# Kernel optimization log

Hardware: AMD Instinct MI355X
Metric: run time of the kernel (lower is better)

Reference implementation:

```python
import jax, jax.numpy as jnp
import numpy as np

# dims (match init_kwargs / input_specs)
K = 2      # sampling size k
B = 4      # batch
V = 2000   # vocab_size == number of graph nodes
D = 64     # embedding_dim
H = 4      # n_heads
DH = 64    # hidden units per head (n_hidden_units[0])
P = 128    # penultimate_hidden_unit
ALPHA = 0.2
NEG = -9e15  # large negative used by GAT to mask non-edges before softmax


def leaky_relu(v):
    return jnp.where(v >= 0, v, ALPHA * v)


def setup_inputs() -> dict:
    key = jax.random.key(0)
    ks = jax.random.split(key, 10)
    x = (jax.random.uniform(ks[0], (K, B, V)) < 0.1).astype(jnp.float32)
    E = jax.random.normal(ks[1], (V, D))                                 # embedding_weight (normal init)
    W = jax.random.normal(ks[2], (H, D, DH)) * (1.0 / np.sqrt(D))        # per-head GAT weight
    a1 = jax.random.normal(ks[3], (H, DH)) * 0.1                         # attention vec, src half
    a2 = jax.random.normal(ks[4], (H, DH)) * 0.1                         # attention vec, dst half
    cls_w = jax.random.normal(ks[5], (H * DH,))                          # cls_weight
    ac1 = jax.random.normal(ks[6], (H * DH,)) * 0.1                      # CLS attention vec halves
    ac2 = jax.random.normal(ks[7], (H * DH,)) * 0.1
    dense_W = jax.random.normal(ks[8], (H * DH, P)) * (1.0 / np.sqrt(H * DH))
    dense_b = jnp.zeros((P,), dtype=jnp.float32)
    return dict(x=x, E=E, W=W, a1=a1, a2=a2, cls_w=cls_w, ac1=ac1, ac2=ac2,
                dense_W=dense_W, dense_b=dense_b)


def gat_block(feat, mask, W, a1, a2):
    # feat: [B,V,Fin], mask: [B,V,V] bool (adj>0 support from outer product)
    Wh = jnp.einsum('bvf,hfo->bhvo', feat, W)                 # [B,H,V,DH]
    f1 = jnp.einsum('bhvo,ho->bhv', Wh, a1)
    f2 = jnp.einsum('bhvo,ho->bhv', Wh, a2)
    e = leaky_relu(f1[:, :, :, None] + f2[:, :, None, :])     # [B,H,V,V]
    e = jnp.where(mask[:, None, :, :], e, NEG)
    attn = jax.nn.softmax(e, axis=-1)
    out = jax.nn.elu(jnp.einsum('bhvu,bhuo->bhvo', attn, Wh))  # concat=True -> elu
    b, h, v, o = out.shape
    return out.transpose(0, 2, 1, 3).reshape(b, v, h * o)      # concat heads -> [B,V,H*DH]


def reference(x, E, W, a1, a2, cls_w, ac1, ac2, dense_W, dense_b):
    latents = [jnp.broadcast_to(cls_w, (B, cls_w.shape[0]))]   # CLS token per sample
    for i in range(K):
        xi = x[i]                                              # [B,V]
        present = xi > 0
        mask = present[:, :, None] & present[:, None, :]       # adj = outer(x,x) > 0
        feat = xi[:, :, None] * E[None]                        # mask embeddings by presence
        feat = gat_block(feat, mask, W, a1, a2)                # single hidden GAT layer
        latent = xi[:, :, None] * feat                         # [B,V,H*DH]
        latents.append(jnp.max(latent, axis=1))                # max-pool over nodes
    h = jnp.stack(latents, axis=1)                             # [B,K+1,F]
    cls = h[:, 0]
    e = leaky_relu((cls @ ac1)[:, None] + h @ ac2)             # [B,K+1]
    attn = jax.nn.softmax(e, axis=-1)
    pooled = jnp.einsum('bk,bkf->bf', attn, h)                 # CLS attention pooling
    return jax.nn.elu(pooled @ dense_W + dense_b)              # activation(dense(.))
```

## Files before the change

### kernel.cpp

```cpp
#include <hip/hip_runtime.h>
#include <hip/hip_bf16.h>

#define KK 2
#define BB 4
#define VV 2000
#define DD 64
#define HH 4
#define DHH 64
#define PP 128
#define ALPHA_ 0.2f

#define RPB 32
#define YB  8

typedef __attribute__((ext_vector_type(8))) short bf16x8;
typedef __attribute__((ext_vector_type(4))) float f32x4;

__device__ __forceinline__ float lrelu(float z) { return fmaxf(z, ALPHA_ * z); }
__device__ __forceinline__ float elu_(float z)  { return z > 0.f ? z : expm1f(z); }
__device__ __forceinline__ short f2bf(float f) {
  __hip_bfloat16 h = __float2bfloat16(f);
  return *reinterpret_cast<short*>(&h);
}

#define OFF_EW   0
#define OFF_F1   512000
#define OFF_F2   520000
#define OFF_LAT  528000
#define OFF_CNT  530048
#define OFF_S    530056

__global__ __launch_bounds__(256) void k_pre(
    const float* __restrict__ E, const float* __restrict__ W,
    const float* __restrict__ a1, const float* __restrict__ a2,
    const float* __restrict__ x,
    float* __restrict__ EW, float* __restrict__ F1, float* __restrict__ F2,
    int* __restrict__ S, int* __restrict__ cnt, float* __restrict__ lat) {
  const int bid = blockIdx.x;
  const int wave = threadIdx.x >> 6, lane = threadIdx.x & 63;
  if (bid < 2000) {
    const int h = bid / 500;
    const int v = (bid % 500) * 4 + wave;
    bool pres = false;
#pragma unroll
    for (int kb = 0; kb < KK * BB; ++kb) pres |= (x[kb * VV + v] > 0.f);
    if (!pres) return;
    const float* Wh = W + h * DD * DHH;
    const float* Ev = E + v * DD;
    float acc = 0.f;
#pragma unroll 8
    for (int d = 0; d < DD; ++d) acc = fmaf(Ev[d], Wh[d * DHH + lane], acc);
    EW[(h * VV + v) * DHH + lane] = acc;
    float r1 = acc * a1[h * DHH + lane];
    float r2 = acc * a2[h * DHH + lane];
#pragma unroll
    for (int s = 32; s; s >>= 1) { r1 += __shfl_xor(r1, s); r2 += __shfl_xor(r2, s); }
    if (lane == 0) { F1[h * VV + v] = r1; F2[h * VV + v] = r2; }
  } else {
    if (wave != 0) return;
    const int kb = bid - 2000;
    for (int i = lane; i < 256; i += 64) lat[kb * 256 + i] = 0.f;
    const float* xr = x + kb * VV;
    int base = 0;
    for (int t = 0; t * 64 < VV; ++t) {
      const int v = t * 64 + lane;
      const bool f = (v < VV) && (xr[v] > 0.f);
      const unsigned long long m = __ballot(f);
      if (f) {
        const int pos = base + __popcll(m & ((1ull << lane) - 1ull));
        S[kb * VV + pos] = v;
      }
      base += __popcll(m);
    }
    if (lane == 0) cnt[kb] = base;
  }
}

__global__ __launch_bounds__(256) void k_attn(
    const float* __restrict__ EW, const float* __restrict__ F1,
    const float* __restrict__ F2, const int* __restrict__ S,
    const int* __restrict__ cnt, float* __restrict__ lat) {
  __shared__ int   Sl[2048];
  __shared__ float G2l[2048];
  __shared__ float G1l[2048];
  __shared__ float SF1[RPB], SM[RPB], SIV[RPB];

  const int kb = blockIdx.x;
  const int h  = blockIdx.z;
  const int tid = threadIdx.x;
  const int wave = tid >> 6, lane = tid & 63;
  const int n = cnt[kb];
  const int nt = (n + RPB - 1) / RPB;
  if ((int)blockIdx.y >= nt) return;
  const int nup = (n + 31) & ~31;

  const int* Skb = S + kb * VV;
  const float* F2h = F2 + h * VV;
  const float* F1h = F1 + h * VV;
  const float* EWh = EW + (size_t)h * VV * DHH;

  for (int j = tid; j < nup; j += 256) {
    const int v = (j < n) ? Skb[j] : Skb[0];
    Sl[j] = v;
    G2l[j] = (j < n) ? F2h[v] : 0.f;
    G1l[j] = F1h[v];
  }
  __syncthreads();

  const int col = (wave << 4) | (lane & 15);
  const int q   = lane >> 4;
  const float* EWcol = EWh + col;

  for (int tile = blockIdx.y; tile < nt; tile += YB) {
    const int r0w = tile * RPB + wave * 8;
    bool act[8]; float f1r[8];
#pragma unroll
    for (int i = 0; i < 8; ++i) {
      const int r = r0w + i;
      act[i] = r < n;
      f1r[i] = G1l[act[i] ? r : 0];
    }
    float m[8];
#pragma unroll
    for (int i = 0; i < 8; ++i) m[i] = -3.4e38f;
    for (int jb = lane; jb < n; jb += 64) {
      const float g = G2l[jb];
#pragma unroll
      for (int i = 0; i < 8; ++i) m[i] = fmaxf(m[i], lrelu(f1r[i] + g));
    }
#pragma unroll
    for (int s = 32; s; s >>= 1)
#pragma unroll
      for (int i = 0; i < 8; ++i) m[i] = fmaxf(m[i], __shfl_xor(m[i], s));
    float sm[8];
#pragma unroll
    for (int i = 0; i < 8; ++i) sm[i] = 0.f;
    for (int jb = lane; jb < n; jb += 64) {
      const float g = G2l[jb];
#pragma unroll
      for (int i = 0; i < 8; ++i) sm[i] += __expf(lrelu(f1r[i] + g) - m[i]);
    }
#pragma unroll
    for (int s = 32; s; s >>= 1)
#pragma unroll
      for (int i = 0; i < 8; ++i) sm[i] += __shfl_xor(sm[i], s);

    __syncthreads();
    if (lane == 0) {
#pragma unroll
      for (int i = 0; i < 8; ++i) {
        SF1[wave * 8 + i] = f1r[i];
        SM[wave * 8 + i]  = m[i];
        SIV[wave * 8 + i] = act[i] ? (1.f / sm[i]) : 0.f;
      }
    }
    __syncthreads();

    const int rl = lane & 15;
    const float f1a = SF1[rl],      ma = SM[rl],      ia = SIV[rl];
    const float f1b = SF1[16 + rl], mb = SM[16 + rl], ib = SIV[16 + rl];
    f32x4 acc0 = {0.f, 0.f, 0.f, 0.f}, acc1 = {0.f, 0.f, 0.f, 0.f};
    for (int kc = 0; kc < nup; kc += 32) {
      const int kq = kc + q * 8;
      const int4 va = *reinterpret_cast<const int4*>(&Sl[kq]);
      const int4 vb = *reinterpret_cast<const int4*>(&Sl[kq + 4]);
      const float4 ga = *reinterpret_cast<const float4*>(&G2l[kq]);
      const float4 gb = *reinterpret_cast<const float4*>(&G2l[kq + 4]);
      float bv[8];
      bv[0] = EWcol[(size_t)va.x * DHH];
      bv[1] = EWcol[(size_t)va.y * DHH];
      bv[2] = EWcol[(size_t)va.z * DHH];
      bv[3] = EWcol[(size_t)va.w * DHH];
      bv[4] = EWcol[(size_t)vb.x * DHH];
      bv[5] = EWcol[(size_t)vb.y * DHH];
      bv[6] = EWcol[(size_t)vb.z * DHH];
      bv[7] = EWcol[(size_t)vb.w * DHH];
      const float g[8] = {ga.x, ga.y, ga.z, ga.w, gb.x, gb.y, gb.z, gb.w};
      float pa[8], pb[8];
#pragma unroll
      for (int t = 0; t < 8; ++t) {
        const float gt = g[t];
        pa[t] = __expf(lrelu(f1a + gt) - ma) * ia;
        pb[t] = __expf(lrelu(f1b + gt) - mb) * ib;
      }
      if (kc + 32 > n) {
#pragma unroll
        for (int t = 0; t < 8; ++t)
          if (kq + t >= n) { pa[t] = 0.f; pb[t] = 0.f; }
      }
      bf16x8 A0, A1, Bf;
#pragma unroll
      for (int t = 0; t < 8; ++t) {
        A0[t] = f2bf(pa[t]);
        A1[t] = f2bf(pb[t]);
        Bf[t] = f2bf(bv[t]);
      }
      acc0 = __builtin_amdgcn_mfma_f32_16x16x32_bf16(A0, Bf, acc0, 0, 0, 0);
      acc1 = __builtin_amdgcn_mfma_f32_16x16x32_bf16(A1, Bf, acc1, 0, 0, 0);
    }
    float vmax = -3.4e38f;
#pragma unroll
    for (int r = 0; r < 4; ++r) {
      const int row0 = tile * RPB + (q << 2) + r;
      const int row1 = row0 + 16;
      if (row0 < n) vmax = fmaxf(vmax, acc0[r]);
      if (row1 < n) vmax = fmaxf(vmax, acc1[r]);
    }
    if (vmax > 0.f)
      atomicMax(reinterpret_cast<int*>(&lat[kb * 256 + h * DHH + col]),
                __float_as_int(vmax));
  }
}

__global__ __launch_bounds__(256) void k_final(
    const float* __restrict__ cls_w, const float* __restrict__ ac1,
    const float* __restrict__ ac2, const float* __restrict__ dW,
    const float* __restrict__ db, const float* __restrict__ lat,
    float* __restrict__ out) {
  const int b = blockIdx.x;
  const int tid = threadIdx.x;
  const int lane = tid & 63, wave = tid >> 6;
  __shared__ float pooled[256];
  __shared__ float red[4][4];
  const float cw = cls_w[tid];
  const float l0 = lat[(0 * BB + b) * 256 + tid];
  const float l1 = lat[(1 * BB + b) * 256 + tid];
  float t0 = cw * ac1[tid];
  float t1 = cw * ac2[tid];
  float t2 = l0 * ac2[tid];
  float t3 = l1 * ac2[tid];
#pragma unroll
  for (int s = 32; s; s >>= 1) {
    t0 += __shfl_xor(t0, s); t1 += __shfl_xor(t1, s);
    t2 += __shfl_xor(t2, s); t3 += __shfl_xor(t3, s);
  }
  if (lane == 0) { red[wave][0] = t0; red[wave][1] = t1; red[wave][2] = t2; red[wave][3] = t3; }
  __syncthreads();
  const float ca1 = red[0][0] + red[1][0] + red[2][0] + red[3][0];
  const float d0  = red[0][1] + red[1][1] + red[2][1] + red[3][1];
  const float d1  = red[0][2] + red[1][2] + red[2][2] + red[3][2];
  const float d2  = red[0][3] + red[1][3] + red[2][3] + red[3][3];
  const float e0 = lrelu(ca1 + d0), e1 = lrelu(ca1 + d1), e2 = lrelu(ca1 + d2);
  const float mm = fmaxf(e0, fmaxf(e1, e2));
  const float x0 = __expf(e0 - mm), x1 = __expf(e1 - mm), x2 = __expf(e2 - mm);
  const float invs = 1.f / (x0 + x1 + x2);
  pooled[tid] = (x0 * cw + x1 * l0 + x2 * l1) * invs;
  __syncthreads();
  if (tid < PP) {
    float acc = db[tid];
    for (int f = 0; f < 256; ++f) acc = fmaf(pooled[f], dW[f * PP + tid], acc);
    out[b * PP + tid] = elu_(acc);
  }
}

extern "C" void kernel_launch(void* const* d_in, const int* in_sizes, int n_in,
                              void* d_out, int out_size, void* d_ws, size_t ws_size,
                              hipStream_t stream) {
  const float* x     = (const float*)d_in[0];
  const float* E     = (const float*)d_in[1];
  const float* W     = (const float*)d_in[2];
  const float* a1    = (const float*)d_in[3];
  const float* a2    = (const float*)d_in[4];
  const float* cls_w = (const float*)d_in[5];
  const float* ac1   = (const float*)d_in[6];
  const float* ac2   = (const float*)d_in[7];
  const float* dW    = (const float*)d_in[8];
  const float* db    = (const float*)d_in[9];
  float* out = (float*)d_out;

  float* ws  = (float*)d_ws;
  float* EW  = ws + OFF_EW;
  float* F1  = ws + OFF_F1;
  float* F2  = ws + OFF_F2;
  float* LAT = ws + OFF_LAT;
  int*   CNT = (int*)(ws + OFF_CNT);
  int*   S   = (int*)(ws + OFF_S);

  k_pre<<<2008, 256, 0, stream>>>(E, W, a1, a2, x, EW, F1, F2, S, CNT, LAT);
  k_attn<<<dim3(KK * BB, YB, HH), 256, 0, stream>>>(EW, F1, F2, S, CNT, LAT);
  k_final<<<BB, 256, 0, stream>>>(cls_w, ac1, ac2, dW, db, LAT, out);
}
```

Measured before the change: 31.68 us.

## Fuse three kernels into one persistent kernel with grid barrier and last-block tail

Merges the precompute, attention and final pooling kernels into a single 256-block launch. A global atomic-counter barrier separates the precompute phase from the attention phase, and the last block to finish (tracked by a second counter) runs the CLS pooling and dense layer. This removes two kernel launch gaps but adds a memset launch, a spin barrier that relies on all 256 blocks being co-resident, and a serialized tail run by a single block.

```diff
diff --git a/kernel.cpp b/kernel.cpp
--- a/kernel.cpp
+++ b/kernel.cpp
@@ -12,6 +12,7 @@
 
 #define RPB 32
 #define YB  8
+#define NBAR 256
 
 typedef __attribute__((ext_vector_type(8))) short bf16x8;
 typedef __attribute__((ext_vector_type(4))) float f32x4;
@@ -29,36 +30,35 @@
 #define OFF_LAT  528000
 #define OFF_CNT  530048
 #define OFF_S    530056
-
-__global__ __launch_bounds__(256) void k_pre(
+#define OFF_CTR  546056
+
+__global__ __launch_bounds__(256, 2) void k_fused(
     const float* __restrict__ E, const float* __restrict__ W,
     const float* __restrict__ a1, const float* __restrict__ a2,
-    const float* __restrict__ x,
+    const float* __restrict__ x, const float* __restrict__ cls_w,
+    const float* __restrict__ ac1, const float* __restrict__ ac2,
+    const float* __restrict__ dW, const float* __restrict__ db,
+    float* __restrict__ out,
     float* __restrict__ EW, float* __restrict__ F1, float* __restrict__ F2,
-    int* __restrict__ S, int* __restrict__ cnt, float* __restrict__ lat) {
+    int* __restrict__ S, int* __restrict__ cnt, float* __restrict__ lat,
+    int* __restrict__ ctr) {
+  __shared__ int   Sl[2048];
+  __shared__ float G2l[2048];
+  __shared__ float G1l[2048];
+  __shared__ float SF1[RPB], SM[RPB], SIV[RPB];
+  __shared__ float pool[4][256];
+  __shared__ int s_last;
+
   const int bid = blockIdx.x;
-  const int wave = threadIdx.x >> 6, lane = threadIdx.x & 63;
-  if (bid < 2000) {
-    const int h = bid / 500;
-    const int v = (bid % 500) * 4 + wave;
-    bool pres = false;
-#pragma unroll
-    for (int kb = 0; kb < KK * BB; ++kb) pres |= (x[kb * VV + v] > 0.f);
-    if (!pres) return;
-    const float* Wh = W + h * DD * DHH;
-    const float* Ev = E + v * DD;
-    float acc = 0.f;
-#pragma unroll 8
-    for (int d = 0; d < DD; ++d) acc = fmaf(Ev[d], Wh[d * DHH + lane], acc);
-    EW[(h * VV + v) * DHH + lane] = acc;
-    float r1 = acc * a1[h * DHH + lane];
-    float r2 = acc * a2[h * DHH + lane];
-#pragma unroll
-    for (int s = 32; s; s >>= 1) { r1 += __shfl_xor(r1, s); r2 += __shfl_xor(r2, s); }
-    if (lane == 0) { F1[h * VV + v] = r1; F2[h * VV + v] = r2; }
-  } else {
-    if (wave != 0) return;
-    const int kb = bid - 2000;
+  const int tid = threadIdx.x;
+  const int wave = tid >> 6, lane = tid & 63;
+
+  const bool do_compact = (bid >= 248);
+  const int g0 = do_compact ? 7936 + (bid - 248) * 8 : bid * 32;
+  const int ng = do_compact ? 8 : 32;
+
+  if (do_compact && wave == 0) {
+    const int kb = bid - 248;
     for (int i = lane; i < 256; i += 64) lat[kb * 256 + i] = 0.f;
     const float* xr = x + kb * VV;
     int base = 0;
@@ -66,191 +66,214 @@
       const int v = t * 64 + lane;
       const bool f = (v < VV) && (xr[v] > 0.f);
       const unsigned long long m = __ballot(f);
-      if (f) {
-        const int pos = base + __popcll(m & ((1ull << lane) - 1ull));
-        S[kb * VV + pos] = v;
-      }
+      if (f) S[kb * VV + base + __popcll(m & ((1ull << lane) - 1ull))] = v;
       base += __popcll(m);
     }
     if (lane == 0) cnt[kb] = base;
-  }
-}
-
-__global__ __launch_bounds__(256) void k_attn(
-    const float* __restrict__ EW, const float* __restrict__ F1,
-    const float* __restrict__ F2, const int* __restrict__ S,
-    const int* __restrict__ cnt, float* __restrict__ lat) {
-  __shared__ int   Sl[2048];
-  __shared__ float G2l[2048];
-  __shared__ float G1l[2048];
-  __shared__ float SF1[RPB], SM[RPB], SIV[RPB];
-
-  const int kb = blockIdx.x;
-  const int h  = blockIdx.z;
-  const int tid = threadIdx.x;
-  const int wave = tid >> 6, lane = tid & 63;
-  const int n = cnt[kb];
+  } else {
+    const int wv = do_compact ? wave - 1 : wave;
+    const int nw = do_compact ? 3 : 4;
+    for (int i = wv; i < ng; i += nw) {
+      const int g = g0 + i;
+      const int h = g / 2000;
+      const int v = g - h * 2000;
+      bool pres = false;
+#pragma unroll
+      for (int kb = 0; kb < KK * BB; ++kb) pres |= (x[kb * VV + v] > 0.f);
+      if (!pres) continue;
+      const float* Wh = W + h * DD * DHH;
+      const float* Ev = E + v * DD;
+      float acc = 0.f;
+#pragma unroll 8
+      for (int d = 0; d < DD; ++d) acc = fmaf(Ev[d], Wh[d * DHH + lane], acc);
+      EW[(size_t)(h * VV + v) * DHH + lane] = acc;
+      float r1 = acc * a1[h * DHH + lane];
+      float r2 = acc * a2[h * DHH + lane];
+#pragma unroll
+      for (int s = 32; s; s >>= 1) { r1 += __shfl_xor(r1, s); r2 += __shfl_xor(r2, s); }
+      if (lane == 0) { F1[h * VV + v] = r1; F2[h * VV + v] = r2; }
+    }
+  }
+
+  __syncthreads();
+  if (tid == 0) {
+    __hip_atomic_fetch_add(&ctr[0], 1, __ATOMIC_ACQ_REL, __HIP_MEMORY_SCOPE_AGENT);
+    while (__hip_atomic_load(&ctr[0], __ATOMIC_ACQUIRE, __HIP_MEMORY_SCOPE_AGENT) < NBAR)
+      __builtin_amdgcn_s_sleep(1);
+  }
+  __syncthreads();
+
+  const int kb = bid & 7;
+  const int y  = (bid >> 3) & 7;
+  const int h  = bid >> 6;
+  const int n  = cnt[kb];
   const int nt = (n + RPB - 1) / RPB;
-  if ((int)blockIdx.y >= nt) return;
-  const int nup = (n + 31) & ~31;
-
-  const int* Skb = S + kb * VV;
-  const float* F2h = F2 + h * VV;
-  const float* F1h = F1 + h * VV;
-  const float* EWh = EW + (size_t)h * VV * DHH;
-
-  for (int j = tid; j < nup; j += 256) {
-    const int v = (j < n) ? Skb[j] : Skb[0];
-    Sl[j] = v;
-    G2l[j] = (j < n) ? F2h[v] : 0.f;
-    G1l[j] = F1h[v];
-  }
-  __syncthreads();
-
-  const int col = (wave << 4) | (lane & 15);
-  const int q   = lane >> 4;
-  const float* EWcol = EWh + col;
-
-  for (int tile = blockIdx.y; tile < nt; tile += YB) {
-    const int r0w = tile * RPB + wave * 8;
-    bool act[8]; float f1r[8];
-#pragma unroll
-    for (int i = 0; i < 8; ++i) {
-      const int r = r0w + i;
-      act[i] = r < n;
-      f1r[i] = G1l[act[i] ? r : 0];
-    }
-    float m[8];
-#pragma unroll
-    for (int i = 0; i < 8; ++i) m[i] = -3.4e38f;
-    for (int jb = lane; jb < n; jb += 64) {
-      const float g = G2l[jb];
-#pragma unroll
-      for (int i = 0; i < 8; ++i) m[i] = fmaxf(m[i], lrelu(f1r[i] + g));
-    }
-#pragma unroll
-    for (int s = 32; s; s >>= 1)
-#pragma unroll
-      for (int i = 0; i < 8; ++i) m[i] = fmaxf(m[i], __shfl_xor(m[i], s));
-    float sm[8];
-#pragma unroll
-    for (int i = 0; i < 8; ++i) sm[i] = 0.f;
-    for (int jb = lane; jb < n; jb += 64) {
-      const float g = G2l[jb];
-#pragma unroll
-      for (int i = 0; i < 8; ++i) sm[i] += __expf(lrelu(f1r[i] + g) - m[i]);
-    }
-#pragma unroll
-    for (int s = 32; s; s >>= 1)
-#pragma unroll
-      for (int i = 0; i < 8; ++i) sm[i] += __shfl_xor(sm[i], s);
-
-    __syncthreads();
-    if (lane == 0) {
-#pragma unroll
-      for (int i = 0; i < 8; ++i) {
-        SF1[wave * 8 + i] = f1r[i];
-        SM[wave * 8 + i]  = m[i];
-        SIV[wave * 8 + i] = act[i] ? (1.f / sm[i]) : 0.f;
-      }
+
+  if (y < nt) {
+    const int nup = (n + 31) & ~31;
+    const int* Skb = S + kb * VV;
+    const float* F2h = F2 + h * VV;
+    const float* F1h = F1 + h * VV;
+    const float* EWh = EW + (size_t)h * VV * DHH;
+
+    for (int j = tid; j < nup; j += 256) {
+      const int v = (j < n) ? Skb[j] : Skb[0];
+      Sl[j] = v;
+      G2l[j] = (j < n) ? F2h[v] : 0.f;
+      G1l[j] = F1h[v];
     }
     __syncthreads();
 
-    const int rl = lane & 15;
-    const float f1a = SF1[rl],      ma = SM[rl],      ia = SIV[rl];
-    const float f1b = SF1[16 + rl], mb = SM[16 + rl], ib = SIV[16 + rl];
-    f32x4 acc0 = {0.f, 0.f, 0.f, 0.f}, acc1 = {0.f, 0.f, 0.f, 0.f};
-    for (int kc = 0; kc < nup; kc += 32) {
-      const int kq = kc + q * 8;
-      const int4 va = *reinterpret_cast<const int4*>(&Sl[kq]);
-      const int4 vb = *reinterpret_cast<const int4*>(&Sl[kq + 4]);
-      const float4 ga = *reinterpret_cast<const float4*>(&G2l[kq]);
-      const float4 gb = *reinterpret_cast<const float4*>(&G2l[kq + 4]);
-      float bv[8];
-      bv[0] = EWcol[(size_t)va.x * DHH];
-      bv[1] = EWcol[(size_t)va.y * DHH];
-      bv[2] = EWcol[(size_t)va.z * DHH];
-      bv[3] = EWcol[(size_t)va.w * DHH];
-      bv[4] = EWcol[(size_t)vb.x * DHH];
-      bv[5] = EWcol[(size_t)vb.y * DHH];
-      bv[6] = EWcol[(size_t)vb.z * DHH];
-      bv[7] = EWcol[(size_t)vb.w * DHH];
-      const float g[8] = {ga.x, ga.y, ga.z, ga.w, gb.x, gb.y, gb.z, gb.w};
-      float pa[8], pb[8];
-#pragma unroll
-      for (int t = 0; t < 8; ++t) {
-        const float gt = g[t];
-        pa[t] = __expf(lrelu(f1a + gt) - ma) * ia;
-        pb[t] = __expf(lrelu(f1b + gt) - mb) * ib;
-      }
-      if (kc + 32 > n) {
-#pragma unroll
-        for (int t = 0; t < 8; ++t)
-          if (kq + t >= n) { pa[t] = 0.f; pb[t] = 0.f; }
-      }
-      bf16x8 A0, A1, Bf;
-#pragma unroll
-      for (int t = 0; t < 8; ++t) {
-        A0[t] = f2bf(pa[t]);
-        A1[t] = f2bf(pb[t]);
-        Bf[t] = f2bf(bv[t]);
-      }
-      acc0 = __builtin_amdgcn_mfma_f32_16x16x32_bf16(A0, Bf, acc0, 0, 0, 0);
-      acc1 = __builtin_amdgcn_mfma_f32_16x16x32_bf16(A1, Bf, acc1, 0, 0, 0);
+    const int col = (wave << 4) | (lane & 15);
+    const int q   = lane >> 4;
+    const float* EWcol = EWh + col;
+
+    for (int tile = y; tile < nt; tile += YB) {
+      const int r0w = tile * RPB + wave * 8;
+      bool act[8]; float f1r[8];
+#pragma unroll
+      for (int i = 0; i < 8; ++i) {
+        const int r = r0w + i;
+        act[i] = r < n;
+        f1r[i] = G1l[act[i] ? r : 0];
+      }
+      float m[8];
+#pragma unroll
+      for (int i = 0; i < 8; ++i) m[i] = -3.4e38f;
+      for (int jb = lane; jb < n; jb += 64) {
+        const float g = G2l[jb];
+#pragma unroll
+        for (int i = 0; i < 8; ++i) m[i] = fmaxf(m[i], lrelu(f1r[i] + g));
+      }
+#pragma unroll
+      for (int s = 32; s; s >>= 1)
+#pragma unroll
+        for (int i = 0; i < 8; ++i) m[i] = fmaxf(m[i], __shfl_xor(m[i], s));
+      float sm[8];
+#pragma unroll
+      for (int i = 0; i < 8; ++i) sm[i] = 0.f;
+      for (int jb = lane; jb < n; jb += 64) {
+        const float g = G2l[jb];
+#pragma unroll
+        for (int i = 0; i < 8; ++i) sm[i] += __expf(lrelu(f1r[i] + g) - m[i]);
+      }
+#pragma unroll
+      for (int s = 32; s; s >>= 1)
+#pragma unroll
+        for (int i = 0; i < 8; ++i) sm[i] += __shfl_xor(sm[i], s);
+
+      __syncthreads();
+      if (lane == 0) {
+#pragma unroll
+        for (int i = 0; i < 8; ++i) {
+          SF1[wave * 8 + i] = f1r[i];
+          SM[wave * 8 + i]  = m[i];
+          SIV[wave * 8 + i] = act[i] ? (1.f / sm[i]) : 0.f;
+        }
+      }
+      __syncthreads();
+
+      const int rl = lane & 15;
+      const float f1a = SF1[rl],      ma = SM[rl],      ia = SIV[rl];
+      const float f1b = SF1[16 + rl], mb = SM[16 + rl], ib = SIV[16 + rl];
+      f32x4 acc0 = {0.f, 0.f, 0.f, 0.f}, acc1 = {0.f, 0.f, 0.f, 0.f};
+      for (int kc = 0; kc < nup; kc += 32) {
+        const int kq = kc + q * 8;
+        const int4 va = *reinterpret_cast<const int4*>(&Sl[kq]);
+        const int4 vb = *reinterpret_cast<const int4*>(&Sl[kq + 4]);
+        const float4 ga = *reinterpret_cast<const float4*>(&G2l[kq]);
+        const float4 gb = *reinterpret_cast<const float4*>(&G2l[kq + 4]);
+        float bv[8];
+        bv[0] = EWcol[(size_t)va.x * DHH];
+        bv[1] = EWcol[(size_t)va.y * DHH];
+        bv[2] = EWcol[(size_t)va.z * DHH];
+        bv[3] = EWcol[(size_t)va.w * DHH];
+        bv[4] = EWcol[(size_t)vb.x * DHH];
+        bv[5] = EWcol[(size_t)vb.y * DHH];
+        bv[6] = EWcol[(size_t)vb.z * DHH];
+        bv[7] = EWcol[(size_t)vb.w * DHH];
+        const float g[8] = {ga.x, ga.y, ga.z, ga.w, gb.x, gb.y, gb.z, gb.w};
+        float pa[8], pb[8];
+#pragma unroll
+        for (int t = 0; t < 8; ++t) {
+          const float gt = g[t];
+          pa[t] = __expf(lrelu(f1a + gt) - ma) * ia;
+          pb[t] = __expf(lrelu(f1b + gt) - mb) * ib;
+        }
+        if (kc + 32 > n) {
+#pragma unroll
+          for (int t = 0; t < 8; ++t)
+            if (kq + t >= n) { pa[t] = 0.f; pb[t] = 0.f; }
+        }
+        bf16x8 A0, A1, Bf;
+#pragma unroll
+        for (int t = 0; t < 8; ++t) {
+          A0[t] = f2bf(pa[t]);
+          A1[t] = f2bf(pb[t]);
+          Bf[t] = f2bf(bv[t]);
+        }
+        acc0 = __builtin_amdgcn_mfma_f32_16x16x32_bf16(A0, Bf, acc0, 0, 0, 0);
+        acc1 = __builtin_amdgcn_mfma_f32_16x16x32_bf16(A1, Bf, acc1, 0, 0, 0);
+      }
+      float vmax = -3.4e38f;
+#pragma unroll
+      for (int r = 0; r < 4; ++r) {
+        const int row0 = tile * RPB + (q << 2) + r;
+        const int row1 = row0 + 16;
+        if (row0 < n) vmax = fmaxf(vmax, acc0[r]);
+        if (row1 < n) vmax = fmaxf(vmax, acc1[r]);
+      }
+      if (vmax > 0.f)
+        atomicMax(reinterpret_cast<int*>(&lat[kb * 256 + h * DHH + col]),
+                  __float_as_int(vmax));
     }
-    float vmax = -3.4e38f;
-#pragma unroll
-    for (int r = 0; r < 4; ++r) {
-      const int row0 = tile * RPB + (q << 2) + r;
-      const int row1 = row0 + 16;
-      if (row0 < n) vmax = fmaxf(vmax, acc0[r]);
-      if (row1 < n) vmax = fmaxf(vmax, acc1[r]);
-    }
-    if (vmax > 0.f)
-      atomicMax(reinterpret_cast<int*>(&lat[kb * 256 + h * DHH + col]),
-                __float_as_int(vmax));
-  }
-}
-
-__global__ __launch_bounds__(256) void k_final(
-    const float* __restrict__ cls_w, const float* __restrict__ ac1,
-    const float* __restrict__ ac2, const float* __restrict__ dW,
-    const float* __restrict__ db, const float* __restrict__ lat,
-    float* __restrict__ out) {
-  const int b = blockIdx.x;
-  const int tid = threadIdx.x;
-  const int lane = tid & 63, wave = tid >> 6;
-  __shared__ float pooled[256];
-  __shared__ float red[4][4];
-  const float cw = cls_w[tid];
-  const float l0 = lat[(0 * BB + b) * 256 + tid];
-  const float l1 = lat[(1 * BB + b) * 256 + tid];
-  float t0 = cw * ac1[tid];
-  float t1 = cw * ac2[tid];
-  float t2 = l0 * ac2[tid];
-  float t3 = l1 * ac2[tid];
+  }
+
+  __syncthreads();
+  if (tid == 0)
+    s_last = (__hip_atomic_fetch_add(&ctr[1], 1, __ATOMIC_ACQ_REL,
+                                     __HIP_MEMORY_SCOPE_AGENT) == NBAR - 1);
+  __syncthreads();
+  if (!s_last) return;
+
+  const int b = wave;
+  float cwv[4], l0v[4], l1v[4];
+  float t0 = 0.f, t1 = 0.f, t2 = 0.f, t3 = 0.f;
+#pragma unroll
+  for (int c = 0; c < 4; ++c) {
+    const int i = lane + 64 * c;
+    const float cw = cls_w[i];
+    const float v1 = ac1[i], v2 = ac2[i];
+    const float l0 = __hip_atomic_load(&lat[(0 * BB + b) * 256 + i],
+                                       __ATOMIC_ACQUIRE, __HIP_MEMORY_SCOPE_AGENT);
+    const float l1 = __hip_atomic_load(&lat[(1 * BB + b) * 256 + i],
+                                       __ATOMIC_ACQUIRE, __HIP_MEMORY_SCOPE_AGENT);
+    cwv[c] = cw; l0v[c] = l0; l1v[c] = l1;
+    t0 += cw * v1; t1 += cw * v2; t2 += l0 * v2; t3 += l1 * v2;
+  }
 #pragma unroll
   for (int s = 32; s; s >>= 1) {
     t0 += __shfl_xor(t0, s); t1 += __shfl_xor(t1, s);
     t2 += __shfl_xor(t2, s); t3 += __shfl_xor(t3, s);
   }
-  if (lane == 0) { red[wave][0] = t0; red[wave][1] = t1; red[wave][2] = t2; red[wave][3] = t3; }
-  __syncthreads();
-  const float ca1 = red[0][0] + red[1][0] + red[2][0] + red[3][0];
-  const float d0  = red[0][1] + red[1][1] + red[2][1] + red[3][1];
-  const float d1  = red[0][2] + red[1][2] + red[2][2] + red[3][2];
-  const float d2  = red[0][3] + red[1][3] + red[2][3] + red[3][3];
-  const float e0 = lrelu(ca1 + d0), e1 = lrelu(ca1 + d1), e2 = lrelu(ca1 + d2);
+  const float e0 = lrelu(t0 + t1), e1 = lrelu(t0 + t2), e2 = lrelu(t0 + t3);
   const float mm = fmaxf(e0, fmaxf(e1, e2));
   const float x0 = __expf(e0 - mm), x1 = __expf(e1 - mm), x2 = __expf(e2 - mm);
   const float invs = 1.f / (x0 + x1 + x2);
-  pooled[tid] = (x0 * cw + x1 * l0 + x2 * l1) * invs;
-  __syncthreads();
-  if (tid < PP) {
-    float acc = db[tid];
-    for (int f = 0; f < 256; ++f) acc = fmaf(pooled[f], dW[f * PP + tid], acc);
-    out[b * PP + tid] = elu_(acc);
-  }
+  const float w0 = x0 * invs, w1 = x1 * invs, w2 = x2 * invs;
+#pragma unroll
+  for (int c = 0; c < 4; ++c)
+    pool[b][lane + 64 * c] = w0 * cwv[c] + w1 * l0v[c] + w2 * l1v[c];
+  __syncthreads();
+  float acc0 = db[lane], acc1 = db[lane + 64];
+#pragma unroll 4
+  for (int f = 0; f < 256; ++f) {
+    const float p = pool[b][f];
+    acc0 = fmaf(p, dW[f * PP + lane], acc0);
+    acc1 = fmaf(p, dW[f * PP + lane + 64], acc1);
+  }
+  out[b * PP + lane] = elu_(acc0);
+  out[b * PP + lane + 64] = elu_(acc1);
 }
 
 extern "C" void kernel_launch(void* const* d_in, const int* in_sizes, int n_in,
@@ -275,8 +298,9 @@
   float* LAT = ws + OFF_LAT;
   int*   CNT = (int*)(ws + OFF_CNT);
   int*   S   = (int*)(ws + OFF_S);
-
-  k_pre<<<2008, 256, 0, stream>>>(E, W, a1, a2, x, EW, F1, F2, S, CNT, LAT);
-  k_attn<<<dim3(KK * BB, YB, HH), 256, 0, stream>>>(EW, F1, F2, S, CNT, LAT);
-  k_final<<<BB, 256, 0, stream>>>(cls_w, ac1, ac2, dW, db, LAT, out);
+  int*   CTR = (int*)(ws + OFF_CTR);
+
+  hipMemsetAsync(CTR, 0, 2 * sizeof(int), stream);
+  k_fused<<<NBAR, 256, 0, stream>>>(E, W, a1, a2, x, cls_w, ac1, ac2, dW, db,
+                                    out, EW, F1, F2, S, CNT, LAT, CTR);
 }
```

After: 68.89 us. 117% more time.

## Fuse final CLS pooling and dense layer into attention kernel via last-block counter

Applied to the files above, without the earlier changes.

Removes the separate k_final launch by having each attention block increment per-(kb,h) and per-batch atomic counters. The last block to finish for a batch runs the CLS attention pooling and dense layer inline, reading the latents with acquire loads. This saves a kernel launch and its dependency gap, but adds a memset launch for the counters plus atomics and an extra barrier in every block.

```diff
diff --git a/kernel.cpp b/kernel.cpp
--- a/kernel.cpp
+++ b/kernel.cpp
@@ -22,6 +22,9 @@
   __hip_bfloat16 h = __float2bfloat16(f);
   return *reinterpret_cast<short*>(&h);
 }
+__device__ __forceinline__ float agent_acq_load(const float* p) {
+  return __hip_atomic_load(p, __ATOMIC_ACQUIRE, __HIP_MEMORY_SCOPE_AGENT);
+}
 
 #define OFF_EW   0
 #define OFF_F1   512000
@@ -29,6 +32,7 @@
 #define OFF_LAT  528000
 #define OFF_CNT  530048
 #define OFF_S    530056
+#define OFF_CTR  546056
 
 __global__ __launch_bounds__(256) void k_pre(
     const float* __restrict__ E, const float* __restrict__ W,
@@ -50,7 +54,7 @@
     float acc = 0.f;
 #pragma unroll 8
     for (int d = 0; d < DD; ++d) acc = fmaf(Ev[d], Wh[d * DHH + lane], acc);
-    EW[(h * VV + v) * DHH + lane] = acc;
+    EW[(size_t)(h * VV + v) * DHH + lane] = acc;
     float r1 = acc * a1[h * DHH + lane];
     float r2 = acc * a2[h * DHH + lane];
 #pragma unroll
@@ -66,10 +70,7 @@
       const int v = t * 64 + lane;
       const bool f = (v < VV) && (xr[v] > 0.f);
       const unsigned long long m = __ballot(f);
-      if (f) {
-        const int pos = base + __popcll(m & ((1ull << lane) - 1ull));
-        S[kb * VV + pos] = v;
-      }
+      if (f) S[kb * VV + base + __popcll(m & ((1ull << lane) - 1ull))] = v;
       base += __popcll(m);
     }
     if (lane == 0) cnt[kb] = base;
@@ -79,11 +80,18 @@
 __global__ __launch_bounds__(256) void k_attn(
     const float* __restrict__ EW, const float* __restrict__ F1,
     const float* __restrict__ F2, const int* __restrict__ S,
-    const int* __restrict__ cnt, float* __restrict__ lat) {
+    const int* __restrict__ cnt, float* __restrict__ lat,
+    const float* __restrict__ cls_w, const float* __restrict__ ac1,
+    const float* __restrict__ ac2, const float* __restrict__ dW,
+    const float* __restrict__ db, float* __restrict__ out,
+    int* __restrict__ ctr) {
   __shared__ int   Sl[2048];
   __shared__ float G2l[2048];
   __shared__ float G1l[2048];
   __shared__ float SF1[RPB], SM[RPB], SIV[RPB];
+  __shared__ float pooled[256];
+  __shared__ float red[4][4];
+  __shared__ int s_fin;
 
   const int kb = blockIdx.x;
   const int h  = blockIdx.z;
@@ -91,140 +99,146 @@
   const int wave = tid >> 6, lane = tid & 63;
   const int n = cnt[kb];
   const int nt = (n + RPB - 1) / RPB;
-  if ((int)blockIdx.y >= nt) return;
-  const int nup = (n + 31) & ~31;
-
-  const int* Skb = S + kb * VV;
-  const float* F2h = F2 + h * VV;
-  const float* F1h = F1 + h * VV;
-  const float* EWh = EW + (size_t)h * VV * DHH;
-
-  for (int j = tid; j < nup; j += 256) {
-    const int v = (j < n) ? Skb[j] : Skb[0];
-    Sl[j] = v;
-    G2l[j] = (j < n) ? F2h[v] : 0.f;
-    G1l[j] = F1h[v];
-  }
-  __syncthreads();
-
-  const int col = (wave << 4) | (lane & 15);
-  const int q   = lane >> 4;
-  const float* EWcol = EWh + col;
-
-  for (int tile = blockIdx.y; tile < nt; tile += YB) {
-    const int r0w = tile * RPB + wave * 8;
-    bool act[8]; float f1r[8];
-#pragma unroll
-    for (int i = 0; i < 8; ++i) {
-      const int r = r0w + i;
-      act[i] = r < n;
-      f1r[i] = G1l[act[i] ? r : 0];
-    }
-    float m[8];
-#pragma unroll
-    for (int i = 0; i < 8; ++i) m[i] = -3.4e38f;
-    for (int jb = lane; jb < n; jb += 64) {
-      const float g = G2l[jb];
-#pragma unroll
-      for (int i = 0; i < 8; ++i) m[i] = fmaxf(m[i], lrelu(f1r[i] + g));
-    }
-#pragma unroll
-    for (int s = 32; s; s >>= 1)
-#pragma unroll
-      for (int i = 0; i < 8; ++i) m[i] = fmaxf(m[i], __shfl_xor(m[i], s));
-    float sm[8];
-#pragma unroll
-    for (int i = 0; i < 8; ++i) sm[i] = 0.f;
-    for (int jb = lane; jb < n; jb += 64) {
-      const float g = G2l[jb];
-#pragma unroll
-      for (int i = 0; i < 8; ++i) sm[i] += __expf(lrelu(f1r[i] + g) - m[i]);
-    }
-#pragma unroll
-    for (int s = 32; s; s >>= 1)
-#pragma unroll
-      for (int i = 0; i < 8; ++i) sm[i] += __shfl_xor(sm[i], s);
-
+
+  if ((int)blockIdx.y < nt) {
+    const int nup = (n + 31) & ~31;
+    const int* Skb = S + kb * VV;
+    const float* F2h = F2 + h * VV;
+    const float* F1h = F1 + h * VV;
+    const float* EWh = EW + (size_t)h * VV * DHH;
+
+    for (int j = tid; j < nup; j += 256) {
+      const int v = (j < n) ? Skb[j] : Skb[0];
+      Sl[j] = v;
+      G2l[j] = (j < n) ? F2h[v] : 0.f;
+      G1l[j] = F1h[v];
+    }
     __syncthreads();
-    if (lane == 0) {
+
+    const int col = (wave << 4) | (lane & 15);
+    const int q   = lane >> 4;
+    const float* EWcol = EWh + col;
+
+    for (int tile = blockIdx.y; tile < nt; tile += YB) {
+      const int r0w = tile * RPB + wave * 8;
+      bool act[8]; float f1r[8];
 #pragma unroll
       for (int i = 0; i < 8; ++i) {
-        SF1[wave * 8 + i] = f1r[i];
-        SM[wave * 8 + i]  = m[i];
-        SIV[wave * 8 + i] = act[i] ? (1.f / sm[i]) : 0.f;
-      }
-    }
-    __syncthreads();
-
-    const int rl = lane & 15;
-    const float f1a = SF1[rl],      ma = SM[rl],      ia = SIV[rl];
-    const float f1b = SF1[16 + rl], mb = SM[16 + rl], ib = SIV[16 + rl];
-    f32x4 acc0 = {0.f, 0.f, 0.f, 0.f}, acc1 = {0.f, 0.f, 0.f, 0.f};
-    for (int kc = 0; kc < nup; kc += 32) {
-      const int kq = kc + q * 8;
-      const int4 va = *reinterpret_cast<const int4*>(&Sl[kq]);
-      const int4 vb = *reinterpret_cast<const int4*>(&Sl[kq + 4]);
-      const float4 ga = *reinterpret_cast<const float4*>(&G2l[kq]);
-      const float4 gb = *reinterpret_cast<const float4*>(&G2l[kq + 4]);
-      float bv[8];
-      bv[0] = EWcol[(size_t)va.x * DHH];
-      bv[1] = EWcol[(size_t)va.y * DHH];
-      bv[2] = EWcol[(size_t)va.z * DHH];
-      bv[3] = EWcol[(size_t)va.w * DHH];
-      bv[4] = EWcol[(size_t)vb.x * DHH];
-      bv[5] = EWcol[(size_t)vb.y * DHH];
-      bv[6] = EWcol[(size_t)vb.z * DHH];
-      bv[7] = EWcol[(size_t)vb.w * DHH];
-      const float g[8] = {ga.x, ga.y, ga.z, ga.w, gb.x, gb.y, gb.z, gb.w};
-      float pa[8], pb[8];
-#pragma unroll
-      for (int t = 0; t < 8; ++t) {
-        const float gt = g[t];
-        pa[t] = __expf(lrelu(f1a + gt) - ma) * ia;
-        pb[t] = __expf(lrelu(f1b + gt) - mb) * ib;
-      }
-      if (kc + 32 > n) {
-#pragma unroll
-        for (int t = 0; t < 8; ++t)
-          if (kq + t >= n) { pa[t] = 0.f; pb[t] = 0.f; }
-      }
-      bf16x8 A0, A1, Bf;
-#pragma unroll
-      for (int t = 0; t < 8; ++t) {
-        A0[t] = f2bf(pa[t]);
-        A1[t] = f2bf(pb[t]);
-        Bf[t] = f2bf(bv[t]);
-      }
-      acc0 = __builtin_amdgcn_mfma_f32_16x16x32_bf16(A0, Bf, acc0, 0, 0, 0);
-      acc1 = __builtin_amdgcn_mfma_f32_16x16x32_bf16(A1, Bf, acc1, 0, 0, 0);
-    }
-    float vmax = -3.4e38f;
-#pragma unroll
-    for (int r = 0; r < 4; ++r) {
-      const int row0 = tile * RPB + (q << 2) + r;
-      const int row1 = row0 + 16;
-      if (row0 < n) vmax = fmaxf(vmax, acc0[r]);
-      if (row1 < n) vmax = fmaxf(vmax, acc1[r]);
-    }
-    if (vmax > 0.f)
-      atomicMax(reinterpret_cast<int*>(&lat[kb * 256 + h * DHH + col]),
-                __float_as_int(vmax));
-  }
-}
-
-__global__ __launch_bounds__(256) void k_final(
-    const float* __restrict__ cls_w, const float* __restrict__ ac1,
-    const float* __restrict__ ac2, const float* __restrict__ dW,
-    const float* __restrict__ db, const float* __restrict__ lat,
-    float* __restrict__ out) {
-  const int b = blockIdx.x;
-  const int tid = threadIdx.x;
-  const int lane = tid & 63, wave = tid >> 6;
-  __shared__ float pooled[256];
-  __shared__ float red[4][4];
+        const int r = r0w + i;
+        act[i] = r < n;
+        f1r[i] = G1l[act[i] ? r : 0];
+      }
+      float m[8];
+#pragma unroll
+      for (int i = 0; i < 8; ++i) m[i] = -3.4e38f;
+      for (int jb = lane; jb < n; jb += 64) {
+        const float g = G2l[jb];
+#pragma unroll
+        for (int i = 0; i < 8; ++i) m[i] = fmaxf(m[i], lrelu(f1r[i] + g));
+      }
+#pragma unroll
+      for (int s = 32; s; s >>= 1)
+#pragma unroll
+        for (int i = 0; i < 8; ++i) m[i] = fmaxf(m[i], __shfl_xor(m[i], s));
+      float sm[8];
+#pragma unroll
+      for (int i = 0; i < 8; ++i) sm[i] = 0.f;
+      for (int jb = lane; jb < n; jb += 64) {
+        const float g = G2l[jb];
+#pragma unroll
+        for (int i = 0; i < 8; ++i) sm[i] += __expf(lrelu(f1r[i] + g) - m[i]);
+      }
+#pragma unroll
+      for (int s = 32; s; s >>= 1)
+#pragma unroll
+        for (int i = 0; i < 8; ++i) sm[i] += __shfl_xor(sm[i], s);
+
+      __syncthreads();
+      if (lane == 0) {
+#pragma unroll
+        for (int i = 0; i < 8; ++i) {
+          SF1[wave * 8 + i] = f1r[i];
+          SM[wave * 8 + i]  = m[i];
+          SIV[wave * 8 + i] = act[i] ? (1.f / sm[i]) : 0.f;
+        }
+      }
+      __syncthreads();
+
+      const int rl = lane & 15;
+      const float f1a = SF1[rl],      ma = SM[rl],      ia = SIV[rl];
+      const float f1b = SF1[16 + rl], mb = SM[16 + rl], ib = SIV[16 + rl];
+      f32x4 acc0 = {0.f, 0.f, 0.f, 0.f}, acc1 = {0.f, 0.f, 0.f, 0.f};
+      for (int kc = 0; kc < nup; kc += 32) {
+        const int kq = kc + q * 8;
+        const int4 va = *reinterpret_cast<const int4*>(&Sl[kq]);
+        const int4 vb = *reinterpret_cast<const int4*>(&Sl[kq + 4]);
+        const float4 ga = *reinterpret_cast<const float4*>(&G2l[kq]);
+        const float4 gb = *reinterpret_cast<const float4*>(&G2l[kq + 4]);
+        float bv[8];
+        bv[0] = EWcol[(size_t)va.x * DHH];
+        bv[1] = EWcol[(size_t)va.y * DHH];
+        bv[2] = EWcol[(size_t)va.z * DHH];
+        bv[3] = EWcol[(size_t)va.w * DHH];
+        bv[4] = EWcol[(size_t)vb.x * DHH];
+        bv[5] = EWcol[(size_t)vb.y * DHH];
+        bv[6] = EWcol[(size_t)vb.z * DHH];
+        bv[7] = EWcol[(size_t)vb.w * DHH];
+        const float g[8] = {ga.x, ga.y, ga.z, ga.w, gb.x, gb.y, gb.z, gb.w};
+        float pa[8], pb[8];
+#pragma unroll
+        for (int t = 0; t < 8; ++t) {
+          const float gt = g[t];
+          pa[t] = __expf(lrelu(f1a + gt) - ma) * ia;
+          pb[t] = __expf(lrelu(f1b + gt) - mb) * ib;
+        }
+        if (kc + 32 > n) {
+#pragma unroll
+          for (int t = 0; t < 8; ++t)
+            if (kq + t >= n) { pa[t] = 0.f; pb[t] = 0.f; }
+        }
+        bf16x8 A0, A1, Bf;
+#pragma unroll
+        for (int t = 0; t < 8; ++t) {
+          A0[t] = f2bf(pa[t]);
+          A1[t] = f2bf(pb[t]);
+          Bf[t] = f2bf(bv[t]);
+        }
+        acc0 = __builtin_amdgcn_mfma_f32_16x16x32_bf16(A0, Bf, acc0, 0, 0, 0);
+        acc1 = __builtin_amdgcn_mfma_f32_16x16x32_bf16(A1, Bf, acc1, 0, 0, 0);
+      }
+      float vmax = -3.4e38f;
+#pragma unroll
+      for (int r = 0; r < 4; ++r) {
+        const int row0 = tile * RPB + (q << 2) + r;
+        const int row1 = row0 + 16;
+        if (row0 < n) vmax = fmaxf(vmax, acc0[r]);
+        if (row1 < n) vmax = fmaxf(vmax, acc1[r]);
+      }
+      if (vmax > 0.f)
+        atomicMax(reinterpret_cast<int*>(&lat[kb * 256 + h * DHH + col]),
+                  __float_as_int(vmax));
+    }
+  }
+
+  __syncthreads();
+  if (tid == 0) {
+    int fin = 0;
+    const int l = __hip_atomic_fetch_add(&ctr[(kb * HH + h) * 16], 1,
+                                         __ATOMIC_ACQ_REL, __HIP_MEMORY_SCOPE_AGENT);
+    if (l == YB - 1) {
+      const int r = __hip_atomic_fetch_add(&ctr[(32 + (kb & 3)) * 16], 1,
+                                           __ATOMIC_ACQ_REL, __HIP_MEMORY_SCOPE_AGENT);
+      fin = (r == KK * HH - 1);
+    }
+    s_fin = fin;
+  }
+  __syncthreads();
+  if (!s_fin) return;
+
+  const int b = kb & 3;
   const float cw = cls_w[tid];
-  const float l0 = lat[(0 * BB + b) * 256 + tid];
-  const float l1 = lat[(1 * BB + b) * 256 + tid];
+  const float l0 = agent_acq_load(&lat[(0 * BB + b) * 256 + tid]);
+  const float l1 = agent_acq_load(&lat[(1 * BB + b) * 256 + tid]);
   float t0 = cw * ac1[tid];
   float t1 = cw * ac2[tid];
   float t2 = l0 * ac2[tid];
@@ -248,6 +262,7 @@
   __syncthreads();
   if (tid < PP) {
     float acc = db[tid];
+#pragma unroll 4
     for (int f = 0; f < 256; ++f) acc = fmaf(pooled[f], dW[f * PP + tid], acc);
     out[b * PP + tid] = elu_(acc);
   }
@@ -275,8 +290,10 @@
   float* LAT = ws + OFF_LAT;
   int*   CNT = (int*)(ws + OFF_CNT);
   int*   S   = (int*)(ws + OFF_S);
-
+  int*   CTR = (int*)(ws + OFF_CTR);
+
+  hipMemsetAsync(CTR, 0, 36 * 16 * sizeof(int), stream);
   k_pre<<<2008, 256, 0, stream>>>(E, W, a1, a2, x, EW, F1, F2, S, CNT, LAT);
-  k_attn<<<dim3(KK * BB, YB, HH), 256, 0, stream>>>(EW, F1, F2, S, CNT, LAT);
-  k_final<<<BB, 256, 0, stream>>>(cls_w, ac1, ac2, dW, db, LAT, out);
-}
+  k_attn<<<dim3(KK * BB, YB, HH), 256, 0, stream>>>(EW, F1, F2, S, CNT, LAT,
+                                                    cls_w, ac1, ac2, dW, db, out, CTR);
+}
```

After: 42.40 us. 33.9% more time.

## Halve attention row tile, double y-blocks, split final dense across threads

Applied to the files above, without the earlier changes.

The attention kernel now handles 16 rows per tile with one MFMA per step instead of 32 rows with two, and launches twice as many y-blocks so more workgroups run in parallel over the roughly 200 active rows. The shared G1 array is dropped and F1 is gathered directly per row. The final dense layer now uses all 256 threads with split-K and multiple accumulators instead of 128 threads running a serial 256-step loop. The trade-off is that each block reloads the full EW gather for fewer rows, so total gather traffic grows.

```diff
diff --git a/kernel.cpp b/kernel.cpp
--- a/kernel.cpp
+++ b/kernel.cpp
@@ -10,8 +10,8 @@
 #define PP 128
 #define ALPHA_ 0.2f
 
-#define RPB 32
-#define YB  8
+#define RPT 16
+#define YT  16
 
 typedef __attribute__((ext_vector_type(8))) short bf16x8;
 typedef __attribute__((ext_vector_type(4))) float f32x4;
@@ -50,7 +50,7 @@
     float acc = 0.f;
 #pragma unroll 8
     for (int d = 0; d < DD; ++d) acc = fmaf(Ev[d], Wh[d * DHH + lane], acc);
-    EW[(h * VV + v) * DHH + lane] = acc;
+    EW[(size_t)(h * VV + v) * DHH + lane] = acc;
     float r1 = acc * a1[h * DHH + lane];
     float r2 = acc * a2[h * DHH + lane];
 #pragma unroll
@@ -66,10 +66,7 @@
       const int v = t * 64 + lane;
       const bool f = (v < VV) && (xr[v] > 0.f);
       const unsigned long long m = __ballot(f);
-      if (f) {
-        const int pos = base + __popcll(m & ((1ull << lane) - 1ull));
-        S[kb * VV + pos] = v;
-      }
+      if (f) S[kb * VV + base + __popcll(m & ((1ull << lane) - 1ull))] = v;
       base += __popcll(m);
     }
     if (lane == 0) cnt[kb] = base;
@@ -82,15 +79,14 @@
     const int* __restrict__ cnt, float* __restrict__ lat) {
   __shared__ int   Sl[2048];
   __shared__ float G2l[2048];
-  __shared__ float G1l[2048];
-  __shared__ float SF1[RPB], SM[RPB], SIV[RPB];
+  __shared__ float SF1[RPT], SM[RPT], SIV[RPT];
 
   const int kb = blockIdx.x;
   const int h  = blockIdx.z;
   const int tid = threadIdx.x;
   const int wave = tid >> 6, lane = tid & 63;
   const int n = cnt[kb];
-  const int nt = (n + RPB - 1) / RPB;
+  const int nt = (n + RPT - 1) / RPT;
   if ((int)blockIdx.y >= nt) return;
   const int nup = (n + 31) & ~31;
 
@@ -103,7 +99,6 @@
     const int v = (j < n) ? Skb[j] : Skb[0];
     Sl[j] = v;
     G2l[j] = (j < n) ? F2h[v] : 0.f;
-    G1l[j] = F1h[v];
   }
   __syncthreads();
 
@@ -111,55 +106,54 @@
   const int q   = lane >> 4;
   const float* EWcol = EWh + col;
 
-  for (int tile = blockIdx.y; tile < nt; tile += YB) {
-    const int r0w = tile * RPB + wave * 8;
-    bool act[8]; float f1r[8];
-#pragma unroll
-    for (int i = 0; i < 8; ++i) {
+  for (int tile = blockIdx.y; tile < nt; tile += YT) {
+    const int r0w = tile * RPT + wave * 4;
+    bool act[4]; float f1r[4];
+#pragma unroll
+    for (int i = 0; i < 4; ++i) {
       const int r = r0w + i;
       act[i] = r < n;
-      f1r[i] = G1l[act[i] ? r : 0];
-    }
-    float m[8];
-#pragma unroll
-    for (int i = 0; i < 8; ++i) m[i] = -3.4e38f;
+      f1r[i] = F1h[Sl[act[i] ? r : 0]];
+    }
+    float m[4];
+#pragma unroll
+    for (int i = 0; i < 4; ++i) m[i] = -3.4e38f;
     for (int jb = lane; jb < n; jb += 64) {
       const float g = G2l[jb];
 #pragma unroll
-      for (int i = 0; i < 8; ++i) m[i] = fmaxf(m[i], lrelu(f1r[i] + g));
+      for (int i = 0; i < 4; ++i) m[i] = fmaxf(m[i], lrelu(f1r[i] + g));
     }
 #pragma unroll
     for (int s = 32; s; s >>= 1)
 #pragma unroll
-      for (int i = 0; i < 8; ++i) m[i] = fmaxf(m[i], __shfl_xor(m[i], s));
-    float sm[8];
-#pragma unroll
-    for (int i = 0; i < 8; ++i) sm[i] = 0.f;
+      for (int i = 0; i < 4; ++i) m[i] = fmaxf(m[i], __shfl_xor(m[i], s));
+    float sm[4];
+#pragma unroll
+    for (int i = 0; i < 4; ++i) sm[i] = 0.f;
     for (int jb = lane; jb < n; jb += 64) {
       const float g = G2l[jb];
 #pragma unroll
-      for (int i = 0; i < 8; ++i) sm[i] += __expf(lrelu(f1r[i] + g) - m[i]);
+      for (int i = 0; i < 4; ++i) sm[i] += __expf(lrelu(f1r[i] + g) - m[i]);
     }
 #pragma unroll
     for (int s = 32; s; s >>= 1)
 #pragma unroll
-      for (int i = 0; i < 8; ++i) sm[i] += __shfl_xor(sm[i], s);
+      for (int i = 0; i < 4; ++i) sm[i] += __shfl_xor(sm[i], s);
 
     __syncthreads();
     if (lane == 0) {
 #pragma unroll
-      for (int i = 0; i < 8; ++i) {
-        SF1[wave * 8 + i] = f1r[i];
-        SM[wave * 8 + i]  = m[i];
-        SIV[wave * 8 + i] = act[i] ? (1.f / sm[i]) : 0.f;
+      for (int i = 0; i < 4; ++i) {
+        SF1[wave * 4 + i] = f1r[i];
+        SM[wave * 4 + i]  = m[i];
+        SIV[wave * 4 + i] = act[i] ? (1.f / sm[i]) : 0.f;
       }
     }
     __syncthreads();
 
     const int rl = lane & 15;
-    const float f1a = SF1[rl],      ma = SM[rl],      ia = SIV[rl];
-    const float f1b = SF1[16 + rl], mb = SM[16 + rl], ib = SIV[16 + rl];
-    f32x4 acc0 = {0.f, 0.f, 0.f, 0.f}, acc1 = {0.f, 0.f, 0.f, 0.f};
+    const float f1a = SF1[rl], ma = SM[rl], ia = SIV[rl];
+    f32x4 acc0 = {0.f, 0.f, 0.f, 0.f};
     for (int kc = 0; kc < nup; kc += 32) {
       const int kq = kc + q * 8;
       const int4 va = *reinterpret_cast<const int4*>(&Sl[kq]);
@@ -176,35 +170,28 @@
       bv[6] = EWcol[(size_t)vb.z * DHH];
       bv[7] = EWcol[(size_t)vb.w * DHH];
       const float g[8] = {ga.x, ga.y, ga.z, ga.w, gb.x, gb.y, gb.z, gb.w};
-      float pa[8], pb[8];
-#pragma unroll
-      for (int t = 0; t < 8; ++t) {
-        const float gt = g[t];
-        pa[t] = __expf(lrelu(f1a + gt) - ma) * ia;
-        pb[t] = __expf(lrelu(f1b + gt) - mb) * ib;
+      float pa[8];
+#pragma unroll
+      for (int t = 0; t < 8; ++t)
+        pa[t] = __expf(lrelu(f1a + g[t]) - ma) * ia;
+      if (kc + 32 > n) {
+#pragma unroll
+        for (int t = 0; t < 8; ++t)
+          if (kq + t >= n) pa[t] = 0.f;
       }
-      if (kc + 32 > n) {
-#pragma unroll
-        for (int t = 0; t < 8; ++t)
-          if (kq + t >= n) { pa[t] = 0.f; pb[t] = 0.f; }
-      }
-      bf16x8 A0, A1, Bf;
+      bf16x8 A0, Bf;
 #pragma unroll
       for (int t = 0; t < 8; ++t) {
         A0[t] = f2bf(pa[t]);
-        A1[t] = f2bf(pb[t]);
         Bf[t] = f2bf(bv[t]);
       }
       acc0 = __builtin_amdgcn_mfma_f32_16x16x32_bf16(A0, Bf, acc0, 0, 0, 0);
-      acc1 = __builtin_amdgcn_mfma_f32_16x16x32_bf16(A1, Bf, acc1, 0, 0, 0);
     }
     float vmax = -3.4e38f;
 #pragma unroll
     for (int r = 0; r < 4; ++r) {
-      const int row0 = tile * RPB + (q << 2) + r;
-      const int row1 = row0 + 16;
+      const int row0 = tile * RPT + (q << 2) + r;
       if (row0 < n) vmax = fmaxf(vmax, acc0[r]);
-      if (row1 < n) vmax = fmaxf(vmax, acc1[r]);
     }
     if (vmax > 0.f)
       atomicMax(reinterpret_cast<int*>(&lat[kb * 256 + h * DHH + col]),
@@ -221,6 +208,7 @@
   const int tid = threadIdx.x;
   const int lane = tid & 63, wave = tid >> 6;
   __shared__ float pooled[256];
+  __shared__ float finp[2][PP];
   __shared__ float red[4][4];
   const float cw = cls_w[tid];
   const float l0 = lat[(0 * BB + b) * 256 + tid];
@@ -246,11 +234,27 @@
   const float invs = 1.f / (x0 + x1 + x2);
   pooled[tid] = (x0 * cw + x1 * l0 + x2 * l1) * invs;
   __syncthreads();
-  if (tid < PP) {
-    float acc = db[tid];
-    for (int f = 0; f < 256; ++f) acc = fmaf(pooled[f], dW[f * PP + tid], acc);
-    out[b * PP + tid] = elu_(acc);
-  }
+  {
+    const int o = tid & (PP - 1), half = tid >> 7;
+    const float* dWc = dW + (half * 128) * PP + o;
+    const float* pl = &pooled[half * 128];
+    float a0 = 0.f, b1 = 0.f, b2 = 0.f, b3 = 0.f;
+    float a4 = 0.f, a5 = 0.f, a6 = 0.f, a7 = 0.f;
+#pragma unroll
+    for (int f = 0; f < 128; f += 8) {
+      a0 = fmaf(pl[f + 0], dWc[(f + 0) * PP], a0);
+      b1 = fmaf(pl[f + 1], dWc[(f + 1) * PP], b1);
+      b2 = fmaf(pl[f + 2], dWc[(f + 2) * PP], b2);
+      b3 = fmaf(pl[f + 3], dWc[(f + 3) * PP], b3);
+      a4 = fmaf(pl[f + 4], dWc[(f + 4) * PP], a4);
+      a5 = fmaf(pl[f + 5], dWc[(f + 5) * PP], a5);
+      a6 = fmaf(pl[f + 6], dWc[(f + 6) * PP], a6);
+      a7 = fmaf(pl[f + 7], dWc[(f + 7) * PP], a7);
+    }
+    finp[half][o] = ((a0 + b1) + (b2 + b3)) + ((a4 + a5) + (a6 + a7));
+  }
+  __syncthreads();
+  if (tid < PP) out[b * PP + tid] = elu_(db[tid] + finp[0][tid] + finp[1][tid]);
 }
 
 extern "C" void kernel_launch(void* const* d_in, const int* in_sizes, int n_in,
@@ -277,6 +281,6 @@
   int*   S   = (int*)(ws + OFF_S);
 
   k_pre<<<2008, 256, 0, stream>>>(E, W, a1, a2, x, EW, F1, F2, S, CNT, LAT);
-  k_attn<<<dim3(KK * BB, YB, HH), 256, 0, stream>>>(EW, F1, F2, S, CNT, LAT);
+  k_attn<<<dim3(KK * BB, YT, HH), 256, 0, stream>>>(EW, F1, F2, S, CNT, LAT);
   k_final<<<BB, 256, 0, stream>>>(cls_w, ac1, ac2, dW, db, LAT, out);
 }
```

New measurement: 34.07 us. 1.08x slower.
